# Performance work log

Measured on AMD Instinct MI355X. Metric: run time of the kernel, lower is better.

Reference implementation:

```python
import jax, jax.numpy as jnp
import numpy as np

DIM = 384
HEADS = 6
POINTS = 4
LEVELS = 3
FFN_DIM = 1024
EPS = 1e-6
SHAPES = [(128, 128), (64, 64), (32, 32)]  # (H, W) per level
B = 4
NQ = 4096


def layer_norm(x, g, b):
    m = jnp.mean(x, axis=-1, keepdims=True)
    v = jnp.mean(jnp.square(x - m), axis=-1, keepdims=True)
    return (x - m) * jax.lax.rsqrt(v + EPS) * g + b


def _bilinear_sample(vl, loc, h, w):
    # vl: [B, heads, Dh, h*w] per-level value; loc: [B, Nq, heads, P, 2] in [0,1]
    # grid_sample(align_corners=False, padding_mode='zeros') semantics
    Bn, Hh, Dh, _ = vl.shape
    Nq, P = loc.shape[1], loc.shape[3]
    x = loc[..., 0] * w - 0.5
    y = loc[..., 1] * h - 0.5
    x0 = jnp.floor(x); y0 = jnp.floor(y)
    wx1 = x - x0; wx0 = 1.0 - wx1
    wy1 = y - y0; wy0 = 1.0 - wy1
    acc = jnp.zeros((Bn, Hh, Dh, Nq, P), dtype=vl.dtype)
    for xi, yi, wgt in ((x0, y0, wx0 * wy0), (x0 + 1, y0, wx1 * wy0),
                        (x0, y0 + 1, wx0 * wy1), (x0 + 1, y0 + 1, wx1 * wy1)):
        valid = (xi >= 0) & (xi <= w - 1) & (yi >= 0) & (yi <= h - 1)
        idx = (jnp.clip(yi, 0, h - 1) * w + jnp.clip(xi, 0, w - 1)).astype(jnp.int32)
        idx = idx.transpose(0, 2, 1, 3).reshape(Bn, Hh, 1, Nq * P)  # [B,heads,1,Nq*P]
        g = jnp.take_along_axis(vl, jnp.broadcast_to(idx, (Bn, Hh, Dh, Nq * P)), axis=3)
        g = g.reshape(Bn, Hh, Dh, Nq, P)
        wm = (wgt * valid.astype(wgt.dtype)).transpose(0, 2, 1, 3)[:, :, None]  # [B,heads,1,Nq,P]
        acc = acc + g * wm
    return acc  # [B, heads, Dh, Nq, P]


def msda(query, value, reference_points, shapes_np, W_off, b_off, W_aw, b_aw, W_v, b_v, W_o, b_o):
    Bn, Nq, D = query.shape
    L = len(shapes_np)
    Dh = D // HEADS
    v = value @ W_v.T + b_v  # [B, Nv, D]
    offsets = (query @ W_off.T + b_off).reshape(Bn, Nq, HEADS, L, POINTS, 2)
    aw = (query @ W_aw.T + b_aw).reshape(Bn, Nq, HEADS, L * POINTS)
    aw = jax.nn.softmax(aw, axis=-1).reshape(Bn, Nq, HEADS, L, POINTS)
    # offset normalizer is [W, H] per level
    norm = jnp.asarray([[w, h] for (h, w) in shapes_np], dtype=query.dtype)
    loc = reference_points[:, :, None, :, None, :] + offsets / norm[None, None, None, :, None, :]
    out = jnp.zeros((Bn, Nq, HEADS, Dh), dtype=query.dtype)
    start = 0
    for l, (h, w) in enumerate(shapes_np):
        vl = v[:, start:start + h * w].reshape(Bn, h * w, HEADS, Dh)
        vl = vl.transpose(0, 2, 3, 1)  # [B, heads, Dh, h*w]
        sampled = _bilinear_sample(vl, loc[:, :, :, l], h, w)  # [B,heads,Dh,Nq,P]
        out = out + jnp.einsum('bhdqp,bqhp->bqhd', sampled, aw[:, :, :, l])
        start += h * w
    return out.reshape(Bn, Nq, D) @ W_o.T + b_o


def setup_inputs():
    key = jax.random.key(0)
    ks = jax.random.split(key, 16)
    nv = sum(h * w for h, w in SHAPES)
    s = 0.02
    f32 = jnp.float32
    return dict(
        query=jax.random.normal(ks[0], (B, NQ, DIM), f32),
        reference_points=jax.random.uniform(ks[1], (B, NQ, LEVELS, 2), f32),
        feat=jax.random.normal(ks[2], (B, nv, DIM), f32),
        spatial_shapes=jnp.asarray(SHAPES, jnp.int32),
        level_start_index=jnp.asarray(np.cumsum([0] + [h * w for h, w in SHAPES])[:-1], jnp.int32),
        qn_g=jnp.ones((DIM,), f32), qn_b=jnp.zeros((DIM,), f32),
        fn_g=jnp.ones((DIM,), f32), fn_b=jnp.zeros((DIM,), f32),
        W_off=jax.random.normal(ks[3], (HEADS * LEVELS * POINTS * 2, DIM), f32) * s,
        b_off=jax.random.normal(ks[4], (HEADS * LEVELS * POINTS * 2,), f32) * s,
        W_aw=jax.random.normal(ks[5], (HEADS * LEVELS * POINTS, DIM), f32) * s,
        b_aw=jnp.zeros((HEADS * LEVELS * POINTS,), f32),
        W_v=jax.random.normal(ks[6], (DIM, DIM), f32) * s, b_v=jnp.zeros((DIM,), f32),
        W_o=jax.random.normal(ks[7], (DIM, DIM), f32) * s, b_o=jnp.zeros((DIM,), f32),
        n1_g=jnp.ones((DIM,), f32), n1_b=jnp.zeros((DIM,), f32),
        W1=jax.random.normal(ks[8], (FFN_DIM, DIM), f32) * s, b1=jnp.zeros((FFN_DIM,), f32),
        W2=jax.random.normal(ks[9], (DIM, FFN_DIM), f32) * s, b2=jnp.zeros((DIM,), f32),
        n2_g=jnp.ones((DIM,), f32), n2_b=jnp.zeros((DIM,), f32),
        gamma=jnp.full((DIM,), 0.01, f32),
    )


def reference(query, reference_points, feat, spatial_shapes, level_start_index,
              qn_g, qn_b, fn_g, fn_b,
              W_off, b_off, W_aw, b_aw, W_v, b_v, W_o, b_o,
              n1_g, n1_b, W1, b1, W2, b2, n2_g, n2_b, gamma):
    shapes_np = [tuple(int(v) for v in row) for row in np.asarray(spatial_shapes)]
    qn = layer_norm(query, qn_g, qn_b)
    fn = layer_norm(feat, fn_g, fn_b)
    # cross_attn (mmcv MSDeformAttn adds identity=query internally, dropout=0)
    x = qn + msda(qn, fn, reference_points, shapes_np,
                  W_off, b_off, W_aw, b_aw, W_v, b_v, W_o, b_o)
    x = layer_norm(x, n1_g, n1_b)
    x = x + (jax.nn.gelu(x @ W1.T + b1) @ W2.T + b2)  # FFN with residual
    x = layer_norm(x, n2_g, n2_b)
    return query + gamma * x
```

## Files before the change

### kernel.cpp

```cpp
#include <hip/hip_runtime.h>
#include <hip/hip_bf16.h>

#define DIMD 384
#define HEADS 6
#define DH 64
#define LEVELS 3
#define POINTS 4
#define FFN 1024
#define BB 4
#define NQ 4096
#define NV 21504
#define MQ (BB*NQ)
#define MV (BB*NV)
#define EPSF 1e-6f

typedef __hip_bfloat16 bf16;
typedef __attribute__((ext_vector_type(8))) short bf16x8;
typedef __attribute__((ext_vector_type(4))) float f32x4;

__device__ __forceinline__ float wave_sum(float v){
  #pragma unroll
  for(int o=32;o;o>>=1) v += __shfl_xor(v,o);
  return v;
}

__global__ __launch_bounds__(256) void prep_k(
  const float* __restrict__ Wv, const float* __restrict__ Wo,
  const float* __restrict__ W1, const float* __restrict__ W2,
  const float* __restrict__ Woff, const float* __restrict__ Waw,
  const float* __restrict__ boff, const float* __restrict__ baw,
  bf16* __restrict__ wv, bf16* __restrict__ wo, bf16* __restrict__ w1,
  bf16* __restrict__ w2, bf16* __restrict__ wcat, float* __restrict__ bcat)
{
  int i = blockIdx.x*256 + threadIdx.x;
  if(i < 147456){ wv[i] = __float2bfloat16(Wv[i]); return; }
  i -= 147456;
  if(i < 147456){ wo[i] = __float2bfloat16(Wo[i]); return; }
  i -= 147456;
  if(i < 393216){ w1[i] = __float2bfloat16(W1[i]); return; }
  i -= 393216;
  if(i < 393216){ w2[i] = __float2bfloat16(W2[i]); return; }
  i -= 393216;
  if(i < 98304){
    int r = i/384, c = i - r*384;
    float v = r<144 ? Woff[r*384+c] : (r<216 ? Waw[(r-144)*384+c] : 0.f);
    wcat[i] = __float2bfloat16(v); return;
  }
  i -= 98304;
  if(i < 256){ bcat[i] = i<144 ? boff[i] : (i<216 ? baw[i-144] : 0.f); }
}

__global__ __launch_bounds__(256) void ln2_k(
    const float* __restrict__ feat, const float* __restrict__ fg,
    const float* __restrict__ fb, bf16* __restrict__ featn,
    const float* __restrict__ query, const float* __restrict__ qg,
    const float* __restrict__ qb, bf16* __restrict__ qn)
{
  const int blk = blockIdx.x;
  const float *x, *g, *b; bf16* o; int row0;
  if(blk < MV/4){ x=feat;  g=fg; b=fb; o=featn; row0 = blk*4; }
  else          { x=query; g=qg; b=qb; o=qn;    row0 = (blk - MV/4)*4; }
  const int row = row0 + (threadIdx.x>>6);
  const int lane = threadIdx.x & 63;
  float vals[6];
  float s=0.f, s2=0.f;
  #pragma unroll
  for(int i=0;i<6;i++){
    float v = x[(size_t)row*DIMD + lane + i*64];
    vals[i]=v; s += v; s2 += v*v;
  }
  s = wave_sum(s); s2 = wave_sum(s2);
  float m = s*(1.f/DIMD);
  float r = rsqrtf(s2*(1.f/DIMD) - m*m + EPSF);
  #pragma unroll
  for(int i=0;i<6;i++){
    int k = lane + i*64;
    o[(size_t)row*DIMD + k] = __float2bfloat16((vals[i]-m)*r*g[k] + b[k]);
  }
}

template<int KK,int MODE,int TM>
__global__ __launch_bounds__(512,2) void gl_k(
    const bf16* __restrict__ A, const bf16* __restrict__ Bw,
    const float* __restrict__ bias, const bf16* __restrict__ res,
    const float* __restrict__ g, const float* __restrict__ b,
    const float* __restrict__ gam, const float* __restrict__ qsrc,
    void* __restrict__ out)
{
  constexpr int MI = TM/16;
  __shared__ __align__(16) short As[64*64];
  __shared__ __align__(16) short Bs[384*64];
  __shared__ float wst[8*64*2];
  __shared__ float st[64*2];
  const int tid = threadIdx.x;
  const int wid = tid>>6, lane = tid&63;
  const int m0 = blockIdx.x*TM;
  const int lr8 = lane>>3, lc8 = (lane&7)*8;
  const int cg = lane>>4;
  f32x4 acc[MI][3] = {};

  for(int k0=0; k0<KK; k0+=64){
    if(wid < TM/8){
      const bf16* srcA = A + (size_t)(m0 + wid*8 + lr8)*KK + k0 + lc8;
      __builtin_amdgcn_global_load_lds((const __attribute__((address_space(1))) void*)srcA,
          (__attribute__((address_space(3))) void*)(As + wid*512), 16, 0, 0);
    }
    #pragma unroll
    for(int u=0;u<6;u++){
      const int t = wid*6 + u;
      const bf16* srcB = Bw + (size_t)(t*8 + lr8)*KK + k0 + lc8;
      __builtin_amdgcn_global_load_lds((const __attribute__((address_space(1))) void*)srcB,
          (__attribute__((address_space(3))) void*)(Bs + t*512), 16, 0, 0);
    }
    asm volatile("s_waitcnt vmcnt(0)" ::: "memory");
    __syncthreads();
    #pragma unroll
    for(int ks=0;ks<2;ks++){
      const int cbase = ks*32 + cg*8;
      bf16x8 af[MI], bfr[3];
      #pragma unroll
      for(int i=0;i<MI;i++)
        af[i] = *(const bf16x8*)(As + (i*16 + (lane&15))*64 + cbase);
      #pragma unroll
      for(int j=0;j<3;j++)
        bfr[j] = *(const bf16x8*)(Bs + (wid*48 + j*16 + (lane&15))*64 + cbase);
      #pragma unroll
      for(int i=0;i<MI;i++)
        #pragma unroll
        for(int j=0;j<3;j++)
          acc[i][j] = __builtin_amdgcn_mfma_f32_16x16x32_bf16(af[i], bfr[j], acc[i][j], 0,0,0);
    }
    __syncthreads();
  }

  if constexpr(MODE == 0){
    #pragma unroll
    for(int i=0;i<MI;i++){
      const int r0 = m0 + i*16 + cg*4;
      #pragma unroll
      for(int j=0;j<3;j++){
        const int col = wid*48 + j*16 + (lane&15);
        const float bv = bias[col];
        #pragma unroll
        for(int rr=0;rr<4;rr++)
          ((bf16*)out)[(size_t)(r0+rr)*DIMD + col] = __float2bfloat16(acc[i][j][rr] + bv);
      }
    }
    return;
  } else {
    float sA[MI][4], sB[MI][4];
    #pragma unroll
    for(int i=0;i<MI;i++)
      #pragma unroll
      for(int rr=0;rr<4;rr++){ sA[i][rr]=0.f; sB[i][rr]=0.f; }
    #pragma unroll
    for(int i=0;i<MI;i++){
      #pragma unroll
      for(int j=0;j<3;j++){
        const int col = wid*48 + j*16 + (lane&15);
        const float bv = bias[col];
        #pragma unroll
        for(int rr=0;rr<4;rr++){
          const int rowg = m0 + i*16 + cg*4 + rr;
          float v = acc[i][j][rr] + bv
                  + __bfloat162float(res[(size_t)rowg*DIMD + col]);
          acc[i][j][rr] = v;
          sA[i][rr] += v; sB[i][rr] += v*v;
        }
      }
    }
    #pragma unroll
    for(int off=1; off<16; off<<=1){
      #pragma unroll
      for(int i=0;i<MI;i++)
        #pragma unroll
        for(int rr=0;rr<4;rr++){
          sA[i][rr] += __shfl_xor(sA[i][rr], off);
          sB[i][rr] += __shfl_xor(sB[i][rr], off);
        }
    }
    if((lane&15)==0){
      #pragma unroll
      for(int i=0;i<MI;i++)
        #pragma unroll
        for(int rr=0;rr<4;rr++){
          const int row = i*16 + cg*4 + rr;
          wst[(wid*TM + row)*2 + 0] = sA[i][rr];
          wst[(wid*TM + row)*2 + 1] = sB[i][rr];
        }
    }
    __syncthreads();
    if(tid < TM){
      float ms=0.f, m2=0.f;
      #pragma unroll
      for(int w=0;w<8;w++){ ms += wst[(w*TM+tid)*2]; m2 += wst[(w*TM+tid)*2+1]; }
      const float m  = ms*(1.f/DIMD);
      const float rs = rsqrtf(m2*(1.f/DIMD) - m*m + EPSF);
      st[tid*2] = m; st[tid*2+1] = rs;
    }
    __syncthreads();
    #pragma unroll
    for(int i=0;i<MI;i++){
      #pragma unroll
      for(int j=0;j<3;j++){
        const int col = wid*48 + j*16 + (lane&15);
        const float gc = g[col], bc = b[col];
        #pragma unroll
        for(int rr=0;rr<4;rr++){
          const int row = i*16 + cg*4 + rr;
          const int rowg = m0 + row;
          const float t = (acc[i][j][rr] - st[row*2])*st[row*2+1]*gc + bc;
          if constexpr(MODE == 1){
            ((bf16*)out)[(size_t)rowg*DIMD + col] = __float2bfloat16(t);
          } else {
            ((float*)out)[(size_t)rowg*DIMD + col] =
                qsrc[(size_t)rowg*DIMD + col] + gam[col]*t;
          }
        }
      }
    }
  }
}

template<int GELU_,int STBF>
__global__ __launch_bounds__(256) void mgemm_k(
    const bf16* __restrict__ A, const bf16* __restrict__ Bw,
    const float* __restrict__ bias, void* __restrict__ Cv,
    int M, int K, int Nreal, int ldc)
{
  __shared__ __align__(16) short As[128*64];
  __shared__ __align__(16) short Bs[128*64];
  const int tid  = threadIdx.x;
  const int wid  = tid>>6, lane = tid&63;
  const int wr   = wid>>1, wc = wid&1;
  const int m0   = blockIdx.y*128, n0 = blockIdx.x*128;
  f32x4 acc[4][4] = {};

  const int sr = (lane>>3);
  const int sc = (lane&7)*8;

  for(int k0=0; k0<K; k0+=64){
    #pragma unroll
    for(int u=0;u<4;u++){
      const int t = wid*4 + u;
      const int r = t*8 + sr;
      const bf16* srcA = A  + (size_t)(m0+r)*K + k0 + sc;
      const bf16* srcB = Bw + (size_t)(n0+r)*K + k0 + sc;
      __builtin_amdgcn_global_load_lds((const __attribute__((address_space(1))) void*)srcA,
          (__attribute__((address_space(3))) void*)(As + t*512), 16, 0, 0);
      __builtin_amdgcn_global_load_lds((const __attribute__((address_space(1))) void*)srcB,
          (__attribute__((address_space(3))) void*)(Bs + t*512), 16, 0, 0);
    }
    asm volatile("s_waitcnt vmcnt(0)" ::: "memory");
    __syncthreads();
    #pragma unroll
    for(int ks=0;ks<2;ks++){
      bf16x8 af[4], bfr[4];
      #pragma unroll
      for(int i=0;i<4;i++){
        const int ar = wr*64 + i*16 + (lane&15);
        af[i]  = *(const bf16x8*)(As + ar*64 + ks*32 + (lane>>4)*8);
        const int br = wc*64 + i*16 + (lane&15);
        bfr[i] = *(const bf16x8*)(Bs + br*64 + ks*32 + (lane>>4)*8);
      }
      #pragma unroll
      for(int i=0;i<4;i++)
        #pragma unroll
        for(int j=0;j<4;j++)
          acc[i][j] = __builtin_amdgcn_mfma_f32_16x16x32_bf16(af[i], bfr[j], acc[i][j], 0,0,0);
    }
    __syncthreads();
  }
  #pragma unroll
  for(int i=0;i<4;i++){
    const int rbase = m0 + wr*64 + i*16 + (lane>>4)*4;
    #pragma unroll
    for(int j=0;j<4;j++){
      const int col = n0 + wc*64 + j*16 + (lane&15);
      if(col >= Nreal) continue;
      const float bv = bias[col];
      #pragma unroll
      for(int rr=0;rr<4;rr++){
        const int rowg = rbase + rr;
        float v = acc[i][j][rr] + bv;
        if constexpr(GELU_){ float u=v; v = 0.5f*u*(1.f+tanhf(0.7978845608028654f*(u+0.044715f*u*u*u))); }
        if constexpr(STBF) ((bf16*)Cv)[(size_t)rowg*ldc + col] = __float2bfloat16(v);
        else               ((float*)Cv)[(size_t)rowg*ldc + col] = v;
      }
    }
  }
}

__global__ __launch_bounds__(256) void msda_k(
    const bf16* __restrict__ v, const float* __restrict__ offaw,
    const float* __restrict__ refp, const int* __restrict__ sshapes,
    const int* __restrict__ lstart, bf16* __restrict__ out)
{
  __shared__ uint2 plds[8][48];
  const int pid0 = blockIdx.x*8;
  const int tid = threadIdx.x;
  if(tid < 96){
    const int pl = tid/12, p12 = tid - pl*12;
    const int pid = pid0 + pl;
    const int bq = pid/6, h = pid - bq*6;
    const int b  = bq >> 12;
    const float* row = offaw + (size_t)bq*216;
    float mx = -1e30f;
    #pragma unroll
    for(int i=0;i<12;i++) mx = fmaxf(mx, row[144 + h*12 + i]);
    float ssum = 0.f, my = 0.f;
    #pragma unroll
    for(int i=0;i<12;i++){
      const float e = __expf(row[144 + h*12 + i] - mx);
      ssum += e;
      if(i==p12) my = e;
    }
    const float aww = my/ssum;
    const int l = p12>>2;
    const int hh = sshapes[2*l], ww = sshapes[2*l+1];
    const int st = lstart[l];
    const float rx = refp[((size_t)bq*LEVELS + l)*2 + 0];
    const float ry = refp[((size_t)bq*LEVELS + l)*2 + 1];
    const float ox = row[(h*12 + p12)*2 + 0];
    const float oy = row[(h*12 + p12)*2 + 1];
    const float px = (rx + ox/(float)ww)*(float)ww - 0.5f;
    const float py = (ry + oy/(float)hh)*(float)hh - 0.5f;
    const float fx0 = floorf(px), fy0 = floorf(py);
    const int x0 = (int)fx0, y0 = (int)fy0;
    const float wx1 = px - fx0, wx0 = 1.f - wx1;
    const float wy1 = py - fy0, wy0 = 1.f - wy1;
    #pragma unroll
    for(int c=0;c<4;c++){
      const int xi = x0 + (c&1);
      const int yi = y0 + (c>>1);
      const float wgt = (c&1 ? wx1 : wx0) * (c>>1 ? wy1 : wy0);
      const bool valid = (xi>=0) & (xi<=ww-1) & (yi>=0) & (yi<=hh-1);
      const int cx = min(max(xi,0), ww-1);
      const int cy = min(max(yi,0), hh-1);
      const unsigned off = (unsigned)((((b*NV + st + cy*ww + cx)*DIMD) + h*DH)*2);
      uint2 pr; pr.x = off; pr.y = __float_as_uint(valid ? wgt*aww : 0.f);
      plds[pl][p12*4 + c] = pr;
    }
  }
  __syncthreads();
  const int pl  = (tid>>5);
  const int pid = pid0 + pl;
  const int ch  = tid & 31;
  const char* vb = (const char*)v;
  float a0 = 0.f, a1 = 0.f;
  #pragma unroll
  for(int c=0;c<48;c++){
    const uint2 pr = plds[pl][c];
    const unsigned g = *(const unsigned*)(vb + pr.x + (ch<<2));
    const float w = __uint_as_float(pr.y);
    a0 = fmaf(w, __uint_as_float(g << 16), a0);
    a1 = fmaf(w, __uint_as_float(g & 0xffff0000u), a1);
  }
  const int bq = pid/6, h = pid - bq*6;
  const unsigned u0 = (unsigned)__builtin_bit_cast(unsigned short, __float2bfloat16(a0));
  const unsigned u1 = (unsigned)__builtin_bit_cast(unsigned short, __float2bfloat16(a1));
  *(unsigned*)((char*)out + (size_t)bq*768 + h*128 + (ch<<2)) = u0 | (u1<<16);
}

static inline size_t rnd(size_t x){ return (x + 511) & ~(size_t)511; }

extern "C" void kernel_launch(void* const* d_in, const int* in_sizes, int n_in,
                              void* d_out, int out_size, void* d_ws, size_t ws_size,
                              hipStream_t stream)
{
  const float* query = (const float*)d_in[0];
  const float* refp  = (const float*)d_in[1];
  const float* feat  = (const float*)d_in[2];
  const int*   sshp  = (const int*)d_in[3];
  const int*   lst   = (const int*)d_in[4];
  const float* qn_g  = (const float*)d_in[5];
  const float* qn_b  = (const float*)d_in[6];
  const float* fn_g  = (const float*)d_in[7];
  const float* fn_b  = (const float*)d_in[8];
  const float* W_off = (const float*)d_in[9];
  const float* b_off = (const float*)d_in[10];
  const float* W_aw  = (const float*)d_in[11];
  const float* b_aw  = (const float*)d_in[12];
  const float* W_v   = (const float*)d_in[13];
  const float* b_v   = (const float*)d_in[14];
  const float* W_o   = (const float*)d_in[15];
  const float* b_o   = (const float*)d_in[16];
  const float* n1_g  = (const float*)d_in[17];
  const float* n1_b  = (const float*)d_in[18];
  const float* W1    = (const float*)d_in[19];
  const float* b1    = (const float*)d_in[20];
  const float* W2    = (const float*)d_in[21];
  const float* b2    = (const float*)d_in[22];
  const float* n2_g  = (const float*)d_in[23];
  const float* n2_b  = (const float*)d_in[24];
  const float* gam   = (const float*)d_in[25];

  char* p = (char*)d_ws;
  bf16* featn = (bf16*)p;
  char* late  = p;
  p += rnd((size_t)MV*DIMD*2);
  bf16* vbuf  = (bf16*)p;  p += rnd((size_t)MV*DIMD*2);
  bf16* qn    = (bf16*)p;  p += rnd((size_t)MQ*DIMD*2);
  bf16* wv    = (bf16*)p;  p += rnd((size_t)147456*2);
  bf16* wo    = (bf16*)p;  p += rnd((size_t)147456*2);
  bf16* w1    = (bf16*)p;  p += rnd((size_t)393216*2);
  bf16* w2    = (bf16*)p;  p += rnd((size_t)393216*2);
  bf16* wcat  = (bf16*)p;  p += rnd((size_t)98304*2);
  float* bcat = (float*)p; p += rnd((size_t)256*4);
  bf16* hbuf  = (bf16*)p;  p += rnd((size_t)MQ*FFN*2);
  char* q2 = late;
  float* offaw = (float*)q2; q2 += rnd((size_t)MQ*216*4);
  bf16*  msda  = (bf16*)q2;  q2 += rnd((size_t)MQ*DIMD*2);
  bf16*  x2    = (bf16*)q2;  q2 += rnd((size_t)MQ*DIMD*2);

  prep_k<<<4609, 256, 0, stream>>>(W_v, W_o, W1, W2, W_off, W_aw, b_off, b_aw,
                                   wv, wo, w1, w2, wcat, bcat);
  ln2_k<<<MV/4 + MQ/4, 256, 0, stream>>>(feat, fn_g, fn_b, featn,
                                         query, qn_g, qn_b, qn);
  gl_k<DIMD,0,64><<<MV/64, 512, 0, stream>>>(featn, wv, b_v, nullptr,
                                             nullptr, nullptr, nullptr, nullptr, vbuf);
  mgemm_k<0,0><<<dim3(2, MQ/128), 256, 0, stream>>>(qn, wcat, bcat, offaw,
                                                    MQ, DIMD, 216, 216);
  msda_k<<<MQ*HEADS/8, 256, 0, stream>>>(vbuf, offaw, refp, sshp, lst, msda);
  gl_k<DIMD,1,32><<<MQ/32, 512, 0, stream>>>(msda, wo, b_o, qn,
                                             n1_g, n1_b, nullptr, nullptr, x2);
  mgemm_k<1,1><<<dim3(8, MQ/128), 256, 0, stream>>>(x2, w1, b1, hbuf,
                                                    MQ, DIMD, FFN, FFN);
  gl_k<FFN,2,32><<<MQ/32, 512, 0, stream>>>(hbuf, w2, b2, x2,
                                            n2_g, n2_b, gam, query, (float*)d_out);
}
```

Before: 257.9 us.

## Merge prep and layernorm launches, co-launch value and offset GEMMs, remap MSDA blocks

Folds the weight-conversion kernel into the dual layernorm kernel, and runs the value projection and the offset/attention-weight projection as one launch with a block-index split. This removes launch gaps and tail effects between small independent stages. The offaw buffer moves out of the aliased late region so it no longer overlaps featn, which both GEMM branches now need live at the same time. The MSDA kernel also gets a block-index swizzle that interleaves query groups across eight strides, presumably to change cache locality or distribution across XCDs.

```diff
diff --git a/kernel.cpp b/kernel.cpp
--- a/kernel.cpp
+++ b/kernel.cpp
@@ -24,42 +24,43 @@
   return v;
 }
 
-__global__ __launch_bounds__(256) void prep_k(
+#define NPREP 4609
+__global__ __launch_bounds__(256) void pre_k(
   const float* __restrict__ Wv, const float* __restrict__ Wo,
   const float* __restrict__ W1, const float* __restrict__ W2,
   const float* __restrict__ Woff, const float* __restrict__ Waw,
   const float* __restrict__ boff, const float* __restrict__ baw,
   bf16* __restrict__ wv, bf16* __restrict__ wo, bf16* __restrict__ w1,
-  bf16* __restrict__ w2, bf16* __restrict__ wcat, float* __restrict__ bcat)
-{
-  int i = blockIdx.x*256 + threadIdx.x;
-  if(i < 147456){ wv[i] = __float2bfloat16(Wv[i]); return; }
-  i -= 147456;
-  if(i < 147456){ wo[i] = __float2bfloat16(Wo[i]); return; }
-  i -= 147456;
-  if(i < 393216){ w1[i] = __float2bfloat16(W1[i]); return; }
-  i -= 393216;
-  if(i < 393216){ w2[i] = __float2bfloat16(W2[i]); return; }
-  i -= 393216;
-  if(i < 98304){
-    int r = i/384, c = i - r*384;
-    float v = r<144 ? Woff[r*384+c] : (r<216 ? Waw[(r-144)*384+c] : 0.f);
-    wcat[i] = __float2bfloat16(v); return;
-  }
-  i -= 98304;
-  if(i < 256){ bcat[i] = i<144 ? boff[i] : (i<216 ? baw[i-144] : 0.f); }
-}
-
-__global__ __launch_bounds__(256) void ln2_k(
-    const float* __restrict__ feat, const float* __restrict__ fg,
-    const float* __restrict__ fb, bf16* __restrict__ featn,
-    const float* __restrict__ query, const float* __restrict__ qg,
-    const float* __restrict__ qb, bf16* __restrict__ qn)
+  bf16* __restrict__ w2, bf16* __restrict__ wcat, float* __restrict__ bcat,
+  const float* __restrict__ feat, const float* __restrict__ fg,
+  const float* __restrict__ fb, bf16* __restrict__ featn,
+  const float* __restrict__ query, const float* __restrict__ qg,
+  const float* __restrict__ qb, bf16* __restrict__ qn)
 {
   const int blk = blockIdx.x;
+  if(blk < NPREP){
+    int i = blk*256 + threadIdx.x;
+    if(i < 147456){ wv[i] = __float2bfloat16(Wv[i]); return; }
+    i -= 147456;
+    if(i < 147456){ wo[i] = __float2bfloat16(Wo[i]); return; }
+    i -= 147456;
+    if(i < 393216){ w1[i] = __float2bfloat16(W1[i]); return; }
+    i -= 393216;
+    if(i < 393216){ w2[i] = __float2bfloat16(W2[i]); return; }
+    i -= 393216;
+    if(i < 98304){
+      int r = i/384, c = i - r*384;
+      float v = r<144 ? Woff[r*384+c] : (r<216 ? Waw[(r-144)*384+c] : 0.f);
+      wcat[i] = __float2bfloat16(v); return;
+    }
+    i -= 98304;
+    if(i < 256){ bcat[i] = i<144 ? boff[i] : (i<216 ? baw[i-144] : 0.f); }
+    return;
+  }
+  const int lblk = blk - NPREP;
   const float *x, *g, *b; bf16* o; int row0;
-  if(blk < MV/4){ x=feat;  g=fg; b=fb; o=featn; row0 = blk*4; }
-  else          { x=query; g=qg; b=qb; o=qn;    row0 = (blk - MV/4)*4; }
+  if(lblk < MV/4){ x=feat;  g=fg; b=fb; o=featn; row0 = lblk*4; }
+  else           { x=query; g=qg; b=qb; o=qn;    row0 = (lblk - MV/4)*4; }
   const int row = row0 + (threadIdx.x>>6);
   const int lane = threadIdx.x & 63;
   float vals[6];
@@ -76,6 +77,121 @@
   for(int i=0;i<6;i++){
     int k = lane + i*64;
     o[(size_t)row*DIMD + k] = __float2bfloat16((vals[i]-m)*r*g[k] + b[k]);
+  }
+}
+
+#define NVB (MV/64)
+__global__ __launch_bounds__(512,2) void gemm2_k(
+    const bf16* __restrict__ A1, const bf16* __restrict__ B1,
+    const float* __restrict__ bias1, bf16* __restrict__ out1,
+    const bf16* __restrict__ A2, const bf16* __restrict__ B2,
+    const float* __restrict__ bias2, float* __restrict__ out2)
+{
+  __shared__ __align__(16) short As[64*64];
+  __shared__ __align__(16) short Bs[384*64];
+  const int tid = threadIdx.x;
+  const int wid = tid>>6, lane = tid&63;
+  const int lr8 = lane>>3, lc8 = (lane&7)*8;
+  const int cg = lane>>4;
+  const bool vbr = blockIdx.x < NVB;
+
+  if(vbr){
+    const int m0 = blockIdx.x*64;
+    f32x4 acc[4][3] = {};
+    for(int k0=0; k0<DIMD; k0+=64){
+      {
+        const bf16* srcA = A1 + (size_t)(m0 + wid*8 + lr8)*DIMD + k0 + lc8;
+        __builtin_amdgcn_global_load_lds((const __attribute__((address_space(1))) void*)srcA,
+            (__attribute__((address_space(3))) void*)(As + wid*512), 16, 0, 0);
+      }
+      #pragma unroll
+      for(int u=0;u<6;u++){
+        const int t = wid*6 + u;
+        const bf16* srcB = B1 + (size_t)(t*8 + lr8)*DIMD + k0 + lc8;
+        __builtin_amdgcn_global_load_lds((const __attribute__((address_space(1))) void*)srcB,
+            (__attribute__((address_space(3))) void*)(Bs + t*512), 16, 0, 0);
+      }
+      asm volatile("s_waitcnt vmcnt(0)" ::: "memory");
+      __syncthreads();
+      #pragma unroll
+      for(int ks=0;ks<2;ks++){
+        const int cbase = ks*32 + cg*8;
+        bf16x8 af[4], bfr[3];
+        #pragma unroll
+        for(int i=0;i<4;i++)
+          af[i] = *(const bf16x8*)(As + (i*16 + (lane&15))*64 + cbase);
+        #pragma unroll
+        for(int j=0;j<3;j++)
+          bfr[j] = *(const bf16x8*)(Bs + (wid*48 + j*16 + (lane&15))*64 + cbase);
+        #pragma unroll
+        for(int i=0;i<4;i++)
+          #pragma unroll
+          for(int j=0;j<3;j++)
+            acc[i][j] = __builtin_amdgcn_mfma_f32_16x16x32_bf16(af[i], bfr[j], acc[i][j], 0,0,0);
+      }
+      __syncthreads();
+    }
+    #pragma unroll
+    for(int i=0;i<4;i++){
+      const int r0 = m0 + i*16 + cg*4;
+      #pragma unroll
+      for(int j=0;j<3;j++){
+        const int col = wid*48 + j*16 + (lane&15);
+        const float bv = bias1[col];
+        #pragma unroll
+        for(int rr=0;rr<4;rr++)
+          out1[(size_t)(r0+rr)*DIMD + col] = __float2bfloat16(acc[i][j][rr] + bv);
+      }
+    }
+  } else {
+    const int m0 = (blockIdx.x - NVB)*64;
+    f32x4 acc[4][2] = {};
+    for(int k0=0; k0<DIMD; k0+=64){
+      {
+        const bf16* srcA = A2 + (size_t)(m0 + wid*8 + lr8)*DIMD + k0 + lc8;
+        __builtin_amdgcn_global_load_lds((const __attribute__((address_space(1))) void*)srcA,
+            (__attribute__((address_space(3))) void*)(As + wid*512), 16, 0, 0);
+      }
+      #pragma unroll
+      for(int u=0;u<4;u++){
+        const int t = wid*4 + u;
+        const bf16* srcB = B2 + (size_t)(t*8 + lr8)*DIMD + k0 + lc8;
+        __builtin_amdgcn_global_load_lds((const __attribute__((address_space(1))) void*)srcB,
+            (__attribute__((address_space(3))) void*)(Bs + t*512), 16, 0, 0);
+      }
+      asm volatile("s_waitcnt vmcnt(0)" ::: "memory");
+      __syncthreads();
+      #pragma unroll
+      for(int ks=0;ks<2;ks++){
+        const int cbase = ks*32 + cg*8;
+        bf16x8 af[4], bfr[2];
+        #pragma unroll
+        for(int i=0;i<4;i++)
+          af[i] = *(const bf16x8*)(As + (i*16 + (lane&15))*64 + cbase);
+        #pragma unroll
+        for(int j=0;j<2;j++)
+          bfr[j] = *(const bf16x8*)(Bs + (wid*32 + j*16 + (lane&15))*64 + cbase);
+        #pragma unroll
+        for(int i=0;i<4;i++)
+          #pragma unroll
+          for(int j=0;j<2;j++)
+            acc[i][j] = __builtin_amdgcn_mfma_f32_16x16x32_bf16(af[i], bfr[j], acc[i][j], 0,0,0);
+      }
+      __syncthreads();
+    }
+    #pragma unroll
+    for(int i=0;i<4;i++){
+      const int r0 = m0 + i*16 + cg*4;
+      #pragma unroll
+      for(int j=0;j<2;j++){
+        const int col = wid*32 + j*16 + (lane&15);
+        if(col >= 216) continue;
+        const float bv = bias2[col];
+        #pragma unroll
+        for(int rr=0;rr<4;rr++)
+          out2[(size_t)(r0+rr)*216 + col] = acc[i][j][rr] + bv;
+      }
+    }
   }
 }
 
@@ -133,89 +249,73 @@
     __syncthreads();
   }
 
-  if constexpr(MODE == 0){
-    #pragma unroll
-    for(int i=0;i<MI;i++){
-      const int r0 = m0 + i*16 + cg*4;
-      #pragma unroll
-      for(int j=0;j<3;j++){
-        const int col = wid*48 + j*16 + (lane&15);
-        const float bv = bias[col];
-        #pragma unroll
-        for(int rr=0;rr<4;rr++)
-          ((bf16*)out)[(size_t)(r0+rr)*DIMD + col] = __float2bfloat16(acc[i][j][rr] + bv);
-      }
-    }
-    return;
-  } else {
-    float sA[MI][4], sB[MI][4];
+  float sA[MI][4], sB[MI][4];
+  #pragma unroll
+  for(int i=0;i<MI;i++)
+    #pragma unroll
+    for(int rr=0;rr<4;rr++){ sA[i][rr]=0.f; sB[i][rr]=0.f; }
+  #pragma unroll
+  for(int i=0;i<MI;i++){
+    #pragma unroll
+    for(int j=0;j<3;j++){
+      const int col = wid*48 + j*16 + (lane&15);
+      const float bv = bias[col];
+      #pragma unroll
+      for(int rr=0;rr<4;rr++){
+        const int rowg = m0 + i*16 + cg*4 + rr;
+        float v = acc[i][j][rr] + bv
+                + __bfloat162float(res[(size_t)rowg*DIMD + col]);
+        acc[i][j][rr] = v;
+        sA[i][rr] += v; sB[i][rr] += v*v;
+      }
+    }
+  }
+  #pragma unroll
+  for(int off=1; off<16; off<<=1){
     #pragma unroll
     for(int i=0;i<MI;i++)
       #pragma unroll
-      for(int rr=0;rr<4;rr++){ sA[i][rr]=0.f; sB[i][rr]=0.f; }
-    #pragma unroll
-    for(int i=0;i<MI;i++){
-      #pragma unroll
-      for(int j=0;j<3;j++){
-        const int col = wid*48 + j*16 + (lane&15);
-        const float bv = bias[col];
-        #pragma unroll
-        for(int rr=0;rr<4;rr++){
-          const int rowg = m0 + i*16 + cg*4 + rr;
-          float v = acc[i][j][rr] + bv
-                  + __bfloat162float(res[(size_t)rowg*DIMD + col]);
-          acc[i][j][rr] = v;
-          sA[i][rr] += v; sB[i][rr] += v*v;
-        }
-      }
-    }
-    #pragma unroll
-    for(int off=1; off<16; off<<=1){
-      #pragma unroll
-      for(int i=0;i<MI;i++)
-        #pragma unroll
-        for(int rr=0;rr<4;rr++){
-          sA[i][rr] += __shfl_xor(sA[i][rr], off);
-          sB[i][rr] += __shfl_xor(sB[i][rr], off);
-        }
-    }
-    if((lane&15)==0){
-      #pragma unroll
-      for(int i=0;i<MI;i++)
-        #pragma unroll
-        for(int rr=0;rr<4;rr++){
-          const int row = i*16 + cg*4 + rr;
-          wst[(wid*TM + row)*2 + 0] = sA[i][rr];
-          wst[(wid*TM + row)*2 + 1] = sB[i][rr];
-        }
-    }
-    __syncthreads();
-    if(tid < TM){
-      float ms=0.f, m2=0.f;
-      #pragma unroll
-      for(int w=0;w<8;w++){ ms += wst[(w*TM+tid)*2]; m2 += wst[(w*TM+tid)*2+1]; }
-      const float m  = ms*(1.f/DIMD);
-      const float rs = rsqrtf(m2*(1.f/DIMD) - m*m + EPSF);
-      st[tid*2] = m; st[tid*2+1] = rs;
-    }
-    __syncthreads();
-    #pragma unroll
-    for(int i=0;i<MI;i++){
-      #pragma unroll
-      for(int j=0;j<3;j++){
-        const int col = wid*48 + j*16 + (lane&15);
-        const float gc = g[col], bc = b[col];
-        #pragma unroll
-        for(int rr=0;rr<4;rr++){
-          const int row = i*16 + cg*4 + rr;
-          const int rowg = m0 + row;
-          const float t = (acc[i][j][rr] - st[row*2])*st[row*2+1]*gc + bc;
-          if constexpr(MODE == 1){
-            ((bf16*)out)[(size_t)rowg*DIMD + col] = __float2bfloat16(t);
-          } else {
-            ((float*)out)[(size_t)rowg*DIMD + col] =
-                qsrc[(size_t)rowg*DIMD + col] + gam[col]*t;
-          }
+      for(int rr=0;rr<4;rr++){
+        sA[i][rr] += __shfl_xor(sA[i][rr], off);
+        sB[i][rr] += __shfl_xor(sB[i][rr], off);
+      }
+  }
+  if((lane&15)==0){
+    #pragma unroll
+    for(int i=0;i<MI;i++)
+      #pragma unroll
+      for(int rr=0;rr<4;rr++){
+        const int row = i*16 + cg*4 + rr;
+        wst[(wid*TM + row)*2 + 0] = sA[i][rr];
+        wst[(wid*TM + row)*2 + 1] = sB[i][rr];
+      }
+  }
+  __syncthreads();
+  if(tid < TM){
+    float ms=0.f, m2=0.f;
+    #pragma unroll
+    for(int w=0;w<8;w++){ ms += wst[(w*TM+tid)*2]; m2 += wst[(w*TM+tid)*2+1]; }
+    const float m  = ms*(1.f/DIMD);
+    const float rs = rsqrtf(m2*(1.f/DIMD) - m*m + EPSF);
+    st[tid*2] = m; st[tid*2+1] = rs;
+  }
+  __syncthreads();
+  #pragma unroll
+  for(int i=0;i<MI;i++){
+    #pragma unroll
+    for(int j=0;j<3;j++){
+      const int col = wid*48 + j*16 + (lane&15);
+      const float gc = g[col], bc = b[col];
+      #pragma unroll
+      for(int rr=0;rr<4;rr++){
+        const int row = i*16 + cg*4 + rr;
+        const int rowg = m0 + row;
+        const float t = (acc[i][j][rr] - st[row*2])*st[row*2+1]*gc + bc;
+        if constexpr(MODE == 1){
+          ((bf16*)out)[(size_t)rowg*DIMD + col] = __float2bfloat16(t);
+        } else {
+          ((float*)out)[(size_t)rowg*DIMD + col] =
+              qsrc[(size_t)rowg*DIMD + col] + gam[col]*t;
         }
       }
     }
@@ -297,7 +397,8 @@
     const int* __restrict__ lstart, bf16* __restrict__ out)
 {
   __shared__ uint2 plds[8][48];
-  const int pid0 = blockIdx.x*8;
+  const int bid = blockIdx.x;
+  const int pid0 = ((bid & 7)*1536 + (bid >> 3))*8;
   const int tid = threadIdx.x;
   if(tid < 96){
     const int pl = tid/12, p12 = tid - pl*12;
@@ -408,19 +509,17 @@
   bf16* wcat  = (bf16*)p;  p += rnd((size_t)98304*2);
   float* bcat = (float*)p; p += rnd((size_t)256*4);
   bf16* hbuf  = (bf16*)p;  p += rnd((size_t)MQ*FFN*2);
+  float* offaw = (float*)p; p += rnd((size_t)MQ*216*4);
   char* q2 = late;
-  float* offaw = (float*)q2; q2 += rnd((size_t)MQ*216*4);
   bf16*  msda  = (bf16*)q2;  q2 += rnd((size_t)MQ*DIMD*2);
   bf16*  x2    = (bf16*)q2;  q2 += rnd((size_t)MQ*DIMD*2);
 
-  prep_k<<<4609, 256, 0, stream>>>(W_v, W_o, W1, W2, W_off, W_aw, b_off, b_aw,
-                                   wv, wo, w1, w2, wcat, bcat);
-  ln2_k<<<MV/4 + MQ/4, 256, 0, stream>>>(feat, fn_g, fn_b, featn,
-                                         query, qn_g, qn_b, qn);
-  gl_k<DIMD,0,64><<<MV/64, 512, 0, stream>>>(featn, wv, b_v, nullptr,
-                                             nullptr, nullptr, nullptr, nullptr, vbuf);
-  mgemm_k<0,0><<<dim3(2, MQ/128), 256, 0, stream>>>(qn, wcat, bcat, offaw,
-                                                    MQ, DIMD, 216, 216);
+  pre_k<<<NPREP + MV/4 + MQ/4, 256, 0, stream>>>(
+      W_v, W_o, W1, W2, W_off, W_aw, b_off, b_aw,
+      wv, wo, w1, w2, wcat, bcat,
+      feat, fn_g, fn_b, featn, query, qn_g, qn_b, qn);
+  gemm2_k<<<NVB + MQ/64, 512, 0, stream>>>(featn, wv, b_v, vbuf,
+                                           qn, wcat, bcat, offaw);
   msda_k<<<MQ*HEADS/8, 256, 0, stream>>>(vbuf, offaw, refp, sshp, lst, msda);
   gl_k<DIMD,1,32><<<MQ/32, 512, 0, stream>>>(msda, wo, b_o, qn,
                                              n1_g, n1_b, nullptr, nullptr, x2);
```

New measurement: 247.0 us. 1.04x faster.
